# Optimization experiments

Hardware: AMD Instinct MI355X
Metric: run time of the kernel (lower is better)

## Reference

```python
import jax, jax.numpy as jnp
import numpy as np

E, A, K = 8192, 128, 512  # parallel_envs, num_agents, passengers per env
P = E * K                 # total passengers (global table rows)


def setup_inputs() -> dict:
    key = jax.random.key(0)
    k1, k2, k3, k4, k5, k6 = jax.random.split(key, 6)
    passengers = jax.random.normal(k1, (P, 11), dtype=jnp.float32)
    # column 0 is the env index of each passenger (used to gather timesteps)
    passengers = passengers.at[:, 0].set(jnp.repeat(jnp.arange(E, dtype=jnp.float32), K))
    accepts = jax.random.bernoulli(k2, 0.5, (E, A))
    picks = jax.random.bernoulli(k3, 0.3, (E, A))
    # env-partitioned global passenger indices: row e targets in [e*K, (e+1)*K)
    local_t = jax.random.randint(k4, (E, A), 0, K, dtype=jnp.int32)
    targets = jnp.arange(E, dtype=jnp.int32)[:, None] * K + local_t
    vectors = jax.random.normal(k5, (E, A, 4), dtype=jnp.float32)
    # give a quarter of agents zero src->dst distance so the pick branch fires
    vectors = vectors.at[:, : A // 4, 2:4].set(vectors[:, : A // 4, 0:2])
    # mark last 8 agent slots per env as invalid (all -100)
    vectors = vectors.at[:, -8:, :].set(-100.0)
    timesteps = jax.random.randint(k6, (E,), 0, 1000, dtype=jnp.int32)
    return {"passengers": passengers, "accepts": accepts, "picks": picks,
            "targets": targets, "vectors": vectors, "timesteps": timesteps}


def _distances(vectors):
    d = jnp.sqrt(((vectors[:, :, 0:2] - vectors[:, :, 2:4]) ** 2).sum(-1))
    return jnp.where((vectors == -100.0).all(-1), jnp.inf, d)


def _dup_mask(t, P):
    # torch: unique(return_inverse, return_counts) -> counts[inverse] > 1 & t != -100
    seg = jnp.where(t >= 0, t, P).ravel()  # -100 -> sentinel bucket P
    counts = jax.ops.segment_sum(jnp.ones(seg.shape, jnp.int32), seg, num_segments=P + 1)
    return (counts[seg].reshape(t.shape) > 1) & (t >= 0)


def reference(passengers, accepts, picks, targets, vectors, timesteps):
    E_, A_ = targets.shape
    P_ = passengers.shape[0]

    distances = _distances(vectors)
    accept_t = jnp.where(accepts, targets, -100)

    def cond(carry):
        t, _ = carry
        return _dup_mask(t, P_).any()

    def body(carry):
        t, d = carry
        dup = _dup_mask(t, P_)
        d = jnp.where(dup, d, jnp.inf)  # cumulative, as in torch
        keep = jnp.arange(A_)[None, :] == jnp.argmin(d, axis=1)[:, None]
        t = jnp.where(dup & ~keep, -100, t)
        return t, d

    accept_t, _ = jax.lax.while_loop(cond, body, (accept_t, distances))

    # scatter accept results into passenger table (at most one agent per passenger now)
    valid = accept_t >= 0
    seg = jnp.where(valid, accept_t, P_).ravel()
    accepted = jax.ops.segment_sum(valid.astype(jnp.int32).ravel(), seg, num_segments=P_ + 1)[:P_] > 0
    agent_ids = jnp.broadcast_to(jnp.arange(A_, dtype=jnp.int32)[None, :], (E_, A_))
    agent_of = jax.ops.segment_max(jnp.where(valid, agent_ids, -100).ravel(), seg, num_segments=P_ + 1)[:P_]
    ts = timesteps[passengers[:, 0].astype(jnp.int32)].astype(passengers.dtype)  # per-passenger timestep

    p = passengers
    p = p.at[:, 6].set(jnp.where(accepted, 1.0, p[:, 6]))
    p = p.at[:, 9].set(jnp.where(accepted, ts, p[:, 9]))
    p = p.at[:, 7].set(jnp.where(accepted, agent_of.astype(p.dtype), p[:, 7]))

    # pick transition: only zero-distance picks succeed
    d2 = _distances(vectors)
    pick_t = jnp.where(picks, targets, -100)
    pd = jnp.where(pick_t >= 0, d2, jnp.inf)
    pick_t = jnp.where(pd < 1e-6, pick_t, -100)
    pvalid = pick_t >= 0
    pseg = jnp.where(pvalid, pick_t, P_).ravel()
    picked = jax.ops.segment_sum(pvalid.astype(jnp.int32).ravel(), pseg, num_segments=P_ + 1)[:P_] > 0
    p = p.at[:, 6].set(jnp.where(picked, 2.0, p[:, 6]))
    p = p.at[:, 10].set(jnp.where(picked, ts, p[:, 10]))
    return p
```

## Files before the change

### kernel.cpp

```cpp
#include <hip/hip_runtime.h>

#define E_ENV  8192
#define A_AG   128
#define K_PASS 512
#define ROW_F  11
#define SLICE_F  (K_PASS * ROW_F)
#define SLICE_V4 (SLICE_F / 4)
#define ITERS    (SLICE_V4 / A_AG)

#define OV_PICK 0x200
#define OV_ACC  0x100

__global__ __launch_bounds__(128) void k_fused(
    const float4* __restrict__ pass4,
    const int*    __restrict__ accepts,
    const int*    __restrict__ picks,
    const int*    __restrict__ targets,
    const float4* __restrict__ vectors,
    const int*    __restrict__ timesteps,
    float4*       __restrict__ out4)
{
    __shared__ float4 slice[SLICE_V4];
    __shared__ int    cnt[K_PASS];
    __shared__ int    ov[K_PASS];
    __shared__ float  swv[2];
    __shared__ int    swi[2];

    const int e   = blockIdx.x;
    const int a   = threadIdx.x;
    const int gid = e * A_AG + a;

    float4 v = vectors[gid];
    const int  t    = targets[gid];
    const bool acc  = accepts[gid] != 0;
    const bool pick = picks[gid] != 0;
    const float tsf = (float)timesteps[e];

    const float4* src = pass4 + (size_t)e * SLICE_V4;
    #pragma unroll
    for (int it = 0; it < ITERS; ++it) {
        const int idx = a + it * A_AG;
        __builtin_amdgcn_global_load_lds(
            (const __attribute__((address_space(1))) void*)(src + idx),
            (__attribute__((address_space(3))) void*)(&slice[idx]),
            16, 0, 0);
    }

    #pragma unroll
    for (int j = 0; j < K_PASS / A_AG; ++j) {
        cnt[a + j * A_AG] = 0;
        ov [a + j * A_AG] = 0;
    }
    __syncthreads();

    bool invalid = (v.x == -100.0f) && (v.y == -100.0f) &&
                   (v.z == -100.0f) && (v.w == -100.0f);
    float dx = v.x - v.z, dy = v.y - v.w;
    float d = sqrtf(dx * dx + dy * dy);
    if (invalid) d = INFINITY;

    const int tl = t - e * K_PASS;

    int at = acc ? t : -100;
    if (at >= 0) atomicAdd(&cnt[tl], 1);
    __syncthreads();

    bool dup = (at >= 0) && (cnt[tl] > 1);
    float bv = dup ? d : INFINITY;
    int   bi = a;

    #pragma unroll
    for (int off = 32; off > 0; off >>= 1) {
        float ovv = __shfl_xor(bv, off);
        int   oii = __shfl_xor(bi, off);
        if (ovv < bv || (ovv == bv && oii < bi)) { bv = ovv; bi = oii; }
    }
    int wave = a >> 6;
    if ((a & 63) == 0) { swv[wave] = bv; swi[wave] = bi; }
    __syncthreads();
    float v0 = swv[0], v1 = swv[1];
    int   i0 = swi[0], i1 = swi[1];
    int bidx = (v1 < v0 || (v1 == v0 && i1 < i0)) ? i1 : i0;

    int f = (dup && a != bidx) ? -100 : at;

    if (f >= 0)            atomicOr(&ov[tl], OV_ACC | a);
    if (pick && d < 1e-6f) atomicOr(&ov[tl], OV_PICK);

    __syncthreads();

    auto patch = [&](float val, unsigned row, int col) -> float {
        int o = ov[row];
        if (col == 6) {
            if (o & OV_PICK) return 2.0f;
            if (o & OV_ACC)  return 1.0f;
        } else if (col == 7) {
            if (o & OV_ACC)  return (float)(o & 0x7f);
        } else if (col == 9) {
            if (o & OV_ACC)  return tsf;
        } else if (col == 10) {
            if (o & OV_PICK) return tsf;
        }
        return val;
    };

    float4* dst = out4 + (size_t)e * SLICE_V4;
    #pragma unroll
    for (int it = 0; it < ITERS; ++it) {
        int idx = a + it * A_AG;
        float4 y = slice[idx];
        unsigned g   = (unsigned)idx * 4u;
        unsigned row = g / 11u;
        int      col = (int)(g - row * 11u);
        y.x = patch(y.x, row, col); if (++col == 11) { col = 0; ++row; }
        y.y = patch(y.y, row, col); if (++col == 11) { col = 0; ++row; }
        y.z = patch(y.z, row, col); if (++col == 11) { col = 0; ++row; }
        y.w = patch(y.w, row, col);
        dst[idx] = y;
    }
}

extern "C" void kernel_launch(void* const* d_in, const int* in_sizes, int n_in,
                              void* d_out, int out_size, void* d_ws, size_t ws_size,
                              hipStream_t stream)
{
    const float* passengers = (const float*)d_in[0];
    const int*   accepts    = (const int*)d_in[1];
    const int*   picks      = (const int*)d_in[2];
    const int*   targets    = (const int*)d_in[3];
    const float* vectors    = (const float*)d_in[4];
    const int*   timesteps  = (const int*)d_in[5];
    float*       out        = (float*)d_out;

    k_fused<<<E_ENV, A_AG, 0, stream>>>(
        (const float4*)passengers, accepts, picks, targets,
        (const float4*)vectors, timesteps, (float4*)out);
}
```

Baseline: 357.1 us.

## Patch passenger rows by scatter into LDS and overlap slice load with dedup

```diff
diff --git a/kernel.cpp b/kernel.cpp
--- a/kernel.cpp
+++ b/kernel.cpp
@@ -8,8 +8,13 @@
 #define SLICE_V4 (SLICE_F / 4)
 #define ITERS    (SLICE_V4 / A_AG)
 
-#define OV_PICK 0x200
-#define OV_ACC  0x100
+
+__device__ __forceinline__ void bar_lds()
+{
+    asm volatile("s_waitcnt lgkmcnt(0)" ::: "memory");
+    __builtin_amdgcn_s_barrier();
+    asm volatile("" ::: "memory");
+}
 
 __global__ __launch_bounds__(128) void k_fused(
     const float4* __restrict__ pass4,
@@ -20,9 +25,8 @@
     const int*    __restrict__ timesteps,
     float4*       __restrict__ out4)
 {
-    __shared__ float4 slice[SLICE_V4];
+    __shared__ float4 slice4[SLICE_V4];
     __shared__ int    cnt[K_PASS];
-    __shared__ int    ov[K_PASS];
     __shared__ float  swv[2];
     __shared__ int    swi[2];
 
@@ -31,27 +35,9 @@
     const int gid = e * A_AG + a;
 
     float4 v = vectors[gid];
-    const int  t    = targets[gid];
-    const bool acc  = accepts[gid] != 0;
-    const bool pick = picks[gid] != 0;
-    const float tsf = (float)timesteps[e];
-
-    const float4* src = pass4 + (size_t)e * SLICE_V4;
-    #pragma unroll
-    for (int it = 0; it < ITERS; ++it) {
-        const int idx = a + it * A_AG;
-        __builtin_amdgcn_global_load_lds(
-            (const __attribute__((address_space(1))) void*)(src + idx),
-            (__attribute__((address_space(3))) void*)(&slice[idx]),
-            16, 0, 0);
-    }
-
-    #pragma unroll
-    for (int j = 0; j < K_PASS / A_AG; ++j) {
-        cnt[a + j * A_AG] = 0;
-        ov [a + j * A_AG] = 0;
-    }
-    __syncthreads();
+    const int t    = targets[gid];
+    const int acc  = accepts[gid];
+    const int pick = picks[gid];
 
     bool invalid = (v.x == -100.0f) && (v.y == -100.0f) &&
                    (v.z == -100.0f) && (v.w == -100.0f);
@@ -60,10 +46,29 @@
     if (invalid) d = INFINITY;
 
     const int tl = t - e * K_PASS;
+    int at = (acc != 0) ? t : -100;
 
-    int at = acc ? t : -100;
+    int mix = t ^ acc ^ pick ^ __float_as_int(d);
+    int z;
+    asm("v_and_b32 %0, 0, %1" : "=v"(z) : "v"(mix));
+
+    const float4* src = pass4 + (size_t)e * SLICE_V4 + z;
+    #pragma unroll
+    for (int it = 0; it < ITERS; ++it) {
+        const int idx = a + it * A_AG;
+        __builtin_amdgcn_global_load_lds(
+            (const __attribute__((address_space(1))) void*)(src + idx),
+            (__attribute__((address_space(3))) void*)(&slice4[idx]),
+            16, 0, 0);
+    }
+
+    #pragma unroll
+    for (int j = 0; j < K_PASS / A_AG; ++j)
+        cnt[a + j * A_AG] = 0;
+    bar_lds();
+
     if (at >= 0) atomicAdd(&cnt[tl], 1);
-    __syncthreads();
+    bar_lds();
 
     bool dup = (at >= 0) && (cnt[tl] > 1);
     float bv = dup ? d : INFINITY;
@@ -71,52 +76,41 @@
 
     #pragma unroll
     for (int off = 32; off > 0; off >>= 1) {
-        float ovv = __shfl_xor(bv, off);
-        int   oii = __shfl_xor(bi, off);
-        if (ovv < bv || (ovv == bv && oii < bi)) { bv = ovv; bi = oii; }
+        float ov = __shfl_xor(bv, off);
+        int   oi = __shfl_xor(bi, off);
+        if (ov < bv || (ov == bv && oi < bi)) { bv = ov; bi = oi; }
     }
     int wave = a >> 6;
     if ((a & 63) == 0) { swv[wave] = bv; swi[wave] = bi; }
-    __syncthreads();
+    bar_lds();
     float v0 = swv[0], v1 = swv[1];
     int   i0 = swi[0], i1 = swi[1];
     int bidx = (v1 < v0 || (v1 == v0 && i1 < i0)) ? i1 : i0;
 
     int f = (dup && a != bidx) ? -100 : at;
 
-    if (f >= 0)            atomicOr(&ov[tl], OV_ACC | a);
-    if (pick && d < 1e-6f) atomicOr(&ov[tl], OV_PICK);
-
     __syncthreads();
 
-    auto patch = [&](float val, unsigned row, int col) -> float {
-        int o = ov[row];
-        if (col == 6) {
-            if (o & OV_PICK) return 2.0f;
-            if (o & OV_ACC)  return 1.0f;
-        } else if (col == 7) {
-            if (o & OV_ACC)  return (float)(o & 0x7f);
-        } else if (col == 9) {
-            if (o & OV_ACC)  return tsf;
-        } else if (col == 10) {
-            if (o & OV_PICK) return tsf;
-        }
-        return val;
-    };
+    float* sliceF = (float*)slice4;
+    const float tsf = (float)timesteps[e];
+
+    if (f >= 0) {
+        sliceF[tl * ROW_F + 6] = 1.0f;
+        sliceF[tl * ROW_F + 7] = (float)a;
+        sliceF[tl * ROW_F + 9] = tsf;
+    }
+    bar_lds();
+    if ((pick != 0) && d < 1e-6f) {
+        sliceF[tl * ROW_F + 6]  = 2.0f;
+        sliceF[tl * ROW_F + 10] = tsf;
+    }
+    bar_lds();
 
     float4* dst = out4 + (size_t)e * SLICE_V4;
     #pragma unroll
     for (int it = 0; it < ITERS; ++it) {
-        int idx = a + it * A_AG;
-        float4 y = slice[idx];
-        unsigned g   = (unsigned)idx * 4u;
-        unsigned row = g / 11u;
-        int      col = (int)(g - row * 11u);
-        y.x = patch(y.x, row, col); if (++col == 11) { col = 0; ++row; }
-        y.y = patch(y.y, row, col); if (++col == 11) { col = 0; ++row; }
-        y.z = patch(y.z, row, col); if (++col == 11) { col = 0; ++row; }
-        y.w = patch(y.w, row, col);
-        dst[idx] = y;
+        const int idx = a + it * A_AG;
+        dst[idx] = slice4[idx];
     }
 }
 
```

Measured after the change: 330.8 us. 1.08x faster.
